# Performance work log

Hardware: AMD Instinct MI355X
Metric: run time of the kernel (lower is better)

Reference implementation:

```python
import jax, jax.numpy as jnp
import numpy as np

B, S, DM = 2, 4096, 512
H, D = 8, 64          # heads, size_per_head
BS = 64               # block size (from == to)
NB = S // BS          # 64 blocks
R = 3                 # num random blocks per middle row


def setup_inputs() -> dict:
    key = jax.random.key(0)
    ks = jax.random.split(key, 8)
    sc = 0.02
    x = jax.random.normal(ks[0], (B, S, DM), dtype=jnp.float32)
    w_q = jax.random.normal(ks[1], (DM, H * D), dtype=jnp.float32) * sc
    b_q = jnp.zeros((H * D,), dtype=jnp.float32)
    w_k = jax.random.normal(ks[2], (DM, H * D), dtype=jnp.float32) * sc
    b_k = jnp.zeros((H * D,), dtype=jnp.float32)
    w_v = jax.random.normal(ks[3], (DM, H * D), dtype=jnp.float32) * sc
    b_v = jnp.zeros((H * D,), dtype=jnp.float32)
    # random attention adjacency: per head, rows 1..NB-2, r random middle blocks
    rand_attn = jax.random.randint(ks[4], (H, NB - 2, R), 1, NB - 1, dtype=jnp.int32)
    return {"x": x, "w_q": w_q, "b_q": b_q, "w_k": w_k, "b_k": b_k,
            "w_v": w_v, "b_v": b_v, "rand_attn": rand_attn}


def _bigbird_attention(q, k, v, rand_attn):
    # q,k,v: [B,H,S,D]; rand_attn: [H,NB-2,R]
    scale = 1.0 / jnp.sqrt(jnp.asarray(D, q.dtype))
    qb = q.reshape(B, H, NB, BS, D)
    kb = k.reshape(B, H, NB, BS, D)
    vb = v.reshape(B, H, NB, BS, D)

    # gather random key/value blocks per head/row: [B,H,NB-2,R*BS,D]
    h_idx = jnp.arange(H)[:, None, None]
    gk = kb[:, h_idx, rand_attn].reshape(B, H, NB - 2, R * BS, D)
    gv = vb[:, h_idx, rand_attn].reshape(B, H, NB - 2, R * BS, D)

    # --- row 0: global, full attention ---
    s0 = jnp.einsum('bhqd,bhkd->bhqk', qb[:, :, 0], k) * scale
    c0 = jnp.einsum('bhqk,bhkd->bhqd', jax.nn.softmax(s0, axis=-1), v)

    # --- row 1: blocks [0,1,2,last] + rand ---
    k1 = jnp.concatenate([kb[:, :, 0], kb[:, :, 1], kb[:, :, 2],
                          kb[:, :, -1], gk[:, :, 0]], axis=2)
    v1 = jnp.concatenate([vb[:, :, 0], vb[:, :, 1], vb[:, :, 2],
                          vb[:, :, -1], gv[:, :, 0]], axis=2)
    s1 = jnp.einsum('bhqd,bhkd->bhqk', qb[:, :, 1], k1) * scale
    c1 = jnp.einsum('bhqk,bhkd->bhqd', jax.nn.softmax(s1, axis=-1), v1)

    # --- middle rows i = 2 .. NB-3: first + band(i-1,i,i+1) + rand + last ---
    q_mid = qb[:, :, 2:NB - 2]                                  # [B,H,M,BS,D]
    band_k = jnp.concatenate([kb[:, :, 1:NB - 3], kb[:, :, 2:NB - 2],
                              kb[:, :, 3:NB - 1]], axis=3)       # [B,H,M,3BS,D]
    band_v = jnp.concatenate([vb[:, :, 1:NB - 3], vb[:, :, 2:NB - 2],
                              vb[:, :, 3:NB - 1]], axis=3)
    gk_mid = gk[:, :, 1:NB - 3]                                  # [B,H,M,R*BS,D]
    gv_mid = gv[:, :, 1:NB - 3]
    s_first = jnp.einsum('bhmqd,bhkd->bhmqk', q_mid, kb[:, :, 0])
    s_band = jnp.einsum('bhmqd,bhmkd->bhmqk', q_mid, band_k)
    s_rand = jnp.einsum('bhmqd,bhmkd->bhmqk', q_mid, gk_mid)
    s_last = jnp.einsum('bhmqd,bhkd->bhmqk', q_mid, kb[:, :, -1])
    s_mid = jnp.concatenate([s_first, s_band, s_rand, s_last], axis=-1) * scale
    p = jax.nn.softmax(s_mid, axis=-1)
    p_first = p[..., :BS]
    p_band = p[..., BS:4 * BS]
    p_rand = p[..., 4 * BS:4 * BS + R * BS]
    p_last = p[..., 4 * BS + R * BS:]
    c_mid = (jnp.einsum('bhmqk,bhkd->bhmqd', p_first, vb[:, :, 0])
             + jnp.einsum('bhmqk,bhmkd->bhmqd', p_band, band_v)
             + jnp.einsum('bhmqk,bhmkd->bhmqd', p_rand, gv_mid)
             + jnp.einsum('bhmqk,bhkd->bhmqd', p_last, vb[:, :, -1]))

    # --- row NB-2: blocks [0, NB-3, NB-2, last] + rand ---
    k2 = jnp.concatenate([kb[:, :, 0], kb[:, :, -3], kb[:, :, -2],
                          kb[:, :, -1], gk[:, :, -1]], axis=2)
    v2 = jnp.concatenate([vb[:, :, 0], vb[:, :, -3], vb[:, :, -2],
                          vb[:, :, -1], gv[:, :, -1]], axis=2)
    s2 = jnp.einsum('bhqd,bhkd->bhqk', qb[:, :, -2], k2) * scale
    c2 = jnp.einsum('bhqk,bhkd->bhqd', jax.nn.softmax(s2, axis=-1), v2)

    # --- last row: global, full attention ---
    s3 = jnp.einsum('bhqd,bhkd->bhqk', qb[:, :, -1], k) * scale
    c3 = jnp.einsum('bhqk,bhkd->bhqd', jax.nn.softmax(s3, axis=-1), v)

    ctx = jnp.concatenate([c0[:, :, None], c1[:, :, None], c_mid,
                           c2[:, :, None], c3[:, :, None]], axis=2)
    return ctx.reshape(B, H, S, D)


def reference(x, w_q, b_q, w_k, b_k, w_v, b_v, rand_attn):
    q = (x @ w_q + b_q).reshape(B, S, H, D).transpose(0, 2, 1, 3)
    k = (x @ w_k + b_k).reshape(B, S, H, D).transpose(0, 2, 1, 3)
    v = (x @ w_v + b_v).reshape(B, S, H, D).transpose(0, 2, 1, 3)
    ctx = _bigbird_attention(q, k, v, rand_attn)  # [B,H,S,D]
    return ctx.transpose(0, 2, 1, 3).reshape(B, S, H * D)
```

## Files before the change

kernel.cpp:

```cpp
#include <hip/hip_runtime.h>
#include <stdint.h>

#define BB 2
#define SS 4096
#define DM 512
#define HH 8
#define DD 64
#define NB 64
#define RR 3

typedef __attribute__((ext_vector_type(8))) short short8;
typedef __attribute__((ext_vector_type(4))) float f4;

__device__ __forceinline__ unsigned short f2bf(float f) {
    unsigned u = __float_as_uint(f);
    unsigned r = (u + 0x7fffu + ((u >> 16) & 1u)) >> 16;
    return (unsigned short)r;
}

__global__ __launch_bounds__(256) void cvt_kernel(
    const float* __restrict__ x,
    const float* __restrict__ wq,
    const float* __restrict__ wk,
    const float* __restrict__ wv,
    unsigned short* __restrict__ xb,
    unsigned short* __restrict__ wbT)
{
    int tid = blockIdx.x * blockDim.x + threadIdx.x;
    const int NX4 = (BB * SS * DM) / 4;
    if (tid < NX4) {
        float4 v = reinterpret_cast<const float4*>(x)[tid];
        ushort4 o;
        o.x = f2bf(v.x); o.y = f2bf(v.y); o.z = f2bf(v.z); o.w = f2bf(v.w);
        reinterpret_cast<ushort4*>(xb)[tid] = o;
    }
    const int NW = 3 * DM * DM;
    if (tid < NW) {
        int n = tid >> 9;
        int k = tid & 511;
        int which = n >> 9;
        int hd = n & 511;
        const float* w = (which == 0) ? wq : (which == 1) ? wk : wv;
        wbT[tid] = f2bf(w[k * DM + hd]);
    }
}

__global__ __launch_bounds__(256) void qkv_gemm(
    const unsigned short* __restrict__ xb,
    const unsigned short* __restrict__ wbT,
    const float* __restrict__ bq,
    const float* __restrict__ bk,
    const float* __restrict__ bv,
    unsigned short* __restrict__ qb,
    unsigned short* __restrict__ kb,
    unsigned short* __restrict__ vT)
{
    __shared__ __attribute__((aligned(16))) unsigned short As[128 * 64];
    __shared__ __attribute__((aligned(16))) unsigned short Bs[128 * 64];
    const int tid = threadIdx.x;
    const int l = tid & 63;
    const int w = tid >> 6;
    const int wr = w >> 1, wc = w & 1;
    const int lq = l & 15, lg = l >> 4;
    const int bid = blockIdx.x;
    const int tn = bid % 12, tm = bid / 12;

    f4 acc[4][4];
#pragma unroll
    for (int m = 0; m < 4; m++)
#pragma unroll
        for (int n = 0; n < 4; n++) acc[m][n] = (f4){0.f, 0.f, 0.f, 0.f};

    for (int kt = 0; kt < 8; ++kt) {
#pragma unroll
        for (int i = 0; i < 4; ++i) {
            int o = i * 4096 + tid * 16;
            int row = o >> 7;
            int g = (o >> 4) & 7;
            short8 va = *reinterpret_cast<const short8*>(
                xb + (size_t)(tm * 128 + row) * DM + kt * 64 + g * 8);
            short8 vb = *reinterpret_cast<const short8*>(
                wbT + (size_t)(tn * 128 + row) * DM + kt * 64 + g * 8);
            int gs = g ^ (row & 7);
            *reinterpret_cast<short8*>(reinterpret_cast<char*>(As) + row * 128 + gs * 16) = va;
            *reinterpret_cast<short8*>(reinterpret_cast<char*>(Bs) + row * 128 + gs * 16) = vb;
        }
        __syncthreads();
#pragma unroll
        for (int c = 0; c < 2; c++) {
            short8 af[4], bf[4];
#pragma unroll
            for (int m = 0; m < 4; m++) {
                int row = wr * 64 + m * 16 + lq;
                int gs = (c * 4 + lg) ^ (row & 7);
                af[m] = *reinterpret_cast<const short8*>(
                    reinterpret_cast<const char*>(As) + row * 128 + gs * 16);
            }
#pragma unroll
            for (int n = 0; n < 4; n++) {
                int row = wc * 64 + n * 16 + lq;
                int gs = (c * 4 + lg) ^ (row & 7);
                bf[n] = *reinterpret_cast<const short8*>(
                    reinterpret_cast<const char*>(Bs) + row * 128 + gs * 16);
            }
#pragma unroll
            for (int m = 0; m < 4; m++)
#pragma unroll
                for (int n = 0; n < 4; n++)
                    acc[m][n] = __builtin_amdgcn_mfma_f32_16x16x32_bf16(af[m], bf[n], acc[m][n], 0, 0, 0);
        }
        __syncthreads();
    }

#pragma unroll
    for (int m = 0; m < 4; m++) {
        int gm = tm * 128 + wr * 64 + m * 16 + lg * 4;
#pragma unroll
        for (int n = 0; n < 4; n++) {
            int gn = tn * 128 + wc * 64 + n * 16 + lq;
            int which = gn >> 9, hd = gn & 511;
            float bias = ((which == 0) ? bq : (which == 1) ? bk : bv)[hd];
            int h = hd >> 6, d = hd & 63;
#pragma unroll
            for (int r = 0; r < 4; r++) {
                int gmr = gm + r;
                int b = gmr >> 12, s = gmr & 4095;
                unsigned short val = f2bf(acc[m][n][r] + bias);
                if (which == 0)
                    qb[(((size_t)b * HH + h) * SS + s) * DD + d] = val;
                else if (which == 1)
                    kb[(((size_t)b * HH + h) * SS + s) * DD + d] = val;
                else
                    vT[(((size_t)b * HH + h) * DD + d) * SS + s] = val;
            }
        }
    }
}

__global__ __launch_bounds__(256) void bigbird_attn(
    const unsigned short* __restrict__ qb,
    const unsigned short* __restrict__ kb,
    const unsigned short* __restrict__ vT,
    const int* __restrict__ rand_attn,
    float* __restrict__ out,
    float* __restrict__ PO,
    float* __restrict__ PL)
{
    __shared__ __attribute__((aligned(16))) unsigned short Kb[2][4096];
    __shared__ __attribute__((aligned(16))) unsigned short Vb[2][4096];
    __shared__ __attribute__((aligned(16))) unsigned short Pl[4][1024];
    const int tid = threadIdx.x;
    const int l = tid & 63, w = tid >> 6;
    const int lq = l & 15, lg = l >> 4;
    const int bid = blockIdx.x;

    int b, h, qi, e = 0, c = 0;
    int kbl[8];
    float bias7 = 0.f;
    bool partial;
    if (bid < 992) {
        partial = false;
        qi = 1 + bid % 62;
        int t = bid / 62;
        h = t & 7;
        b = t >> 3;
        kbl[0] = 0;
        if (qi == 1)       { kbl[1] = 1;  kbl[2] = 2;  kbl[3] = 63; }
        else if (qi == 62) { kbl[1] = 61; kbl[2] = 62; kbl[3] = 63; }
        else               { kbl[1] = qi - 1; kbl[2] = qi; kbl[3] = qi + 1; }
        const int* ra = rand_attn + (h * 62 + (qi - 1)) * 3;
        kbl[4] = ra[0]; kbl[5] = ra[1]; kbl[6] = ra[2];
        if (qi == 1 || qi == 62) { kbl[7] = 0; bias7 = -30.f; }
        else kbl[7] = 63;
    } else {
        partial = true;
        int idx = bid - 992;
        c = idx & 7;
        e = (idx >> 3) & 1;
        h = (idx >> 4) & 7;
        b = idx >> 7;
        qi = e ? 63 : 0;
#pragma unroll
        for (int i = 0; i < 8; ++i) kbl[i] = c * 8 + i;
    }

    const size_t bh = (size_t)b * HH + h;
    const unsigned short* qp = qb + bh * SS * DD;
    const char* kpB = reinterpret_cast<const char*>(kb + bh * SS * DD);
    const char* vpB = reinterpret_cast<const char*>(vT + bh * (size_t)DD * SS);

    const int qrow = qi * 64 + w * 16 + lq;
    short8 qf[2];
#pragma unroll
    for (int cc = 0; cc < 2; cc++)
        qf[cc] = *reinterpret_cast<const short8*>(qp + (size_t)qrow * DD + cc * 32 + lg * 8);

    const int r0 = tid >> 3;
    const int sg = tid & 7;
    const int swz0 = (sg ^ (r0 & 7)) << 4;

#define STAGE_LOAD(blk)                                                                 \
    st0 = *reinterpret_cast<const short8*>(kpB + (size_t)(blk) * 8192 + r0 * 128 + sg * 16);        \
    st1 = *reinterpret_cast<const short8*>(kpB + (size_t)(blk) * 8192 + (r0 + 32) * 128 + sg * 16); \
    st2 = *reinterpret_cast<const short8*>(vpB + (size_t)r0 * 8192 + (size_t)(blk) * 128 + sg * 16);\
    st3 = *reinterpret_cast<const short8*>(vpB + (size_t)(r0 + 32) * 8192 + (size_t)(blk) * 128 + sg * 16);

#define STAGE_WRITE(bb)                                                                  \
    *reinterpret_cast<short8*>(reinterpret_cast<char*>(Kb[bb]) + r0 * 128 + swz0) = st0;             \
    *reinterpret_cast<short8*>(reinterpret_cast<char*>(Kb[bb]) + (r0 + 32) * 128 + swz0) = st1;      \
    *reinterpret_cast<short8*>(reinterpret_cast<char*>(Vb[bb]) + r0 * 128 + swz0) = st2;             \
    *reinterpret_cast<short8*>(reinterpret_cast<char*>(Vb[bb]) + (r0 + 32) * 128 + swz0) = st3;

    short8 st0, st1, st2, st3;
    STAGE_LOAD(kbl[0]);
    STAGE_WRITE(0);
    __syncthreads();

    float lacc[4] = {0.f, 0.f, 0.f, 0.f};
    f4 oacc[4];
#pragma unroll
    for (int g = 0; g < 4; g++) oacc[g] = (f4){0.f, 0.f, 0.f, 0.f};

    char* pb = reinterpret_cast<char*>(&Pl[w][0]);
    const float scale = 0.125f;

#pragma unroll
    for (int i = 0; i < 8; ++i) {
        const int cur = i & 1, nxt = cur ^ 1;
        if (i < 7) { STAGE_LOAD(kbl[i + 1]); }
        const float bi = (i == 7) ? bias7 : 0.f;
        const char* Kc = reinterpret_cast<const char*>(Kb[cur]);
        const char* Vc = reinterpret_cast<const char*>(Vb[cur]);

        f4 sacc[4];
#pragma unroll
        for (int g = 0; g < 4; g++) sacc[g] = (f4){0.f, 0.f, 0.f, 0.f};
#pragma unroll
        for (int cc = 0; cc < 2; cc++) {
#pragma unroll
            for (int g = 0; g < 4; g++) {
                int row = g * 16 + lq;
                short8 kf = *reinterpret_cast<const short8*>(
                    Kc + row * 128 + (((cc * 4 + lg) ^ (row & 7)) << 4));
                sacc[g] = __builtin_amdgcn_mfma_f32_16x16x32_bf16(qf[cc], kf, sacc[g], 0, 0, 0);
            }
        }

#pragma unroll
        for (int g = 0; g < 4; g++)
#pragma unroll
            for (int r = 0; r < 4; r++) {
                float pv = __expf(fmaf(sacc[g][r], scale, bi));
                lacc[r] += pv;
                int row = lg * 4 + r;
                int colbyte = (g * 16 + lq) * 2;
                int gr = (colbyte >> 4) ^ (row & 7);
                *reinterpret_cast<unsigned short*>(pb + row * 128 + (gr << 4) + (colbyte & 15)) =
                    f2bf(pv);
            }

        short8 pa[2];
#pragma unroll
        for (int cc = 0; cc < 2; cc++) {
            int row = lq;
            int gr = (cc * 4 + lg) ^ (row & 7);
            pa[cc] = *reinterpret_cast<const short8*>(pb + row * 128 + (gr << 4));
        }

#pragma unroll
        for (int cc = 0; cc < 2; cc++)
#pragma unroll
            for (int g = 0; g < 4; g++) {
                int row = g * 16 + lq;
                short8 vf = *reinterpret_cast<const short8*>(
                    Vc + row * 128 + (((cc * 4 + lg) ^ (row & 7)) << 4));
                oacc[g] = __builtin_amdgcn_mfma_f32_16x16x32_bf16(pa[cc], vf, oacc[g], 0, 0, 0);
            }

        __syncthreads();
        if (i < 7) { STAGE_WRITE(nxt); }
        __syncthreads();
    }

#pragma unroll
    for (int off = 1; off < 16; off <<= 1)
#pragma unroll
        for (int r = 0; r < 4; r++) lacc[r] += __shfl_xor(lacc[r], off, 64);

    if (!partial) {
#pragma unroll
        for (int r = 0; r < 4; r++) {
            float inv = 1.0f / lacc[r];
            int row = lg * 4 + r;
            int s = qi * 64 + w * 16 + row;
#pragma unroll
            for (int g = 0; g < 4; g++) {
                int d = g * 16 + lq;
                out[((size_t)b * SS + s) * DM + h * DD + d] = oacc[g][r] * inv;
            }
        }
    } else {
        int pr = ((b * 8 + h) * 2 + e);
        float* po = PO + ((size_t)(pr * 8 + c) << 12);
        float* pl = PL + (pr * 8 + c) * 64;
#pragma unroll
        for (int r = 0; r < 4; r++) {
            int row = w * 16 + lg * 4 + r;
#pragma unroll
            for (int g = 0; g < 4; g++)
                po[row * 64 + g * 16 + lq] = oacc[g][r];
            if (lq == 0) pl[row] = lacc[r];
        }
    }
#undef STAGE_LOAD
#undef STAGE_WRITE
}

__global__ __launch_bounds__(256) void bigbird_combine(
    const float* __restrict__ PO,
    const float* __restrict__ PL,
    float* __restrict__ out)
{
    int pr = blockIdx.x;
    int e = pr & 1, h = (pr >> 1) & 7, b = pr >> 4;
    int t = threadIdx.x;
    int row = t >> 2;
    int d0 = (t & 3) * 16;

    float acc[16];
#pragma unroll
    for (int j = 0; j < 16; j++) acc[j] = 0.f;
    float lsum = 0.f;

#pragma unroll
    for (int c = 0; c < 8; c++) {
        const float* po = PO + ((size_t)(pr * 8 + c) << 12) + row * 64 + d0;
#pragma unroll
        for (int j = 0; j < 4; j++) {
            float4 v = *reinterpret_cast<const float4*>(po + j * 4);
            acc[j * 4 + 0] += v.x; acc[j * 4 + 1] += v.y;
            acc[j * 4 + 2] += v.z; acc[j * 4 + 3] += v.w;
        }
        lsum += PL[(pr * 8 + c) * 64 + row];
    }

    int qi = e ? 63 : 0;
    int s = qi * 64 + row;
    float inv = 1.0f / lsum;
    float* op = out + ((size_t)b * SS + s) * DM + h * DD + d0;
#pragma unroll
    for (int j = 0; j < 4; j++) {
        float4 v;
        v.x = acc[j * 4 + 0] * inv; v.y = acc[j * 4 + 1] * inv;
        v.z = acc[j * 4 + 2] * inv; v.w = acc[j * 4 + 3] * inv;
        *reinterpret_cast<float4*>(op + j * 4) = v;
    }
}

extern "C" void kernel_launch(void* const* d_in, const int* in_sizes, int n_in,
                              void* d_out, int out_size, void* d_ws, size_t ws_size,
                              hipStream_t stream) {
    const float* x  = (const float*)d_in[0];
    const float* wq = (const float*)d_in[1];
    const float* bq = (const float*)d_in[2];
    const float* wk = (const float*)d_in[3];
    const float* bk = (const float*)d_in[4];
    const float* wv = (const float*)d_in[5];
    const float* bv = (const float*)d_in[6];
    const int* rand_attn = (const int*)d_in[7];
    float* out = (float*)d_out;

    char* ws = (char*)d_ws;
    unsigned short* xb  = (unsigned short*)ws;
    unsigned short* wbT = (unsigned short*)(ws + 8388608);
    unsigned short* qbp = (unsigned short*)(ws + 9961472);
    unsigned short* kbp = qbp + (size_t)4194304;
    unsigned short* vTp = kbp + (size_t)4194304;
    float* PO = (float*)(ws + 35127296);
    float* PL = (float*)(ws + 35127296 + 4194304);

    hipLaunchKernelGGL(cvt_kernel, dim3(4096), dim3(256), 0, stream, x, wq, wk, wv, xb, wbT);
    hipLaunchKernelGGL(qkv_gemm, dim3(768), dim3(256), 0, stream, xb, wbT, bq, bk, bv, qbp, kbp, vTp);
    hipLaunchKernelGGL(bigbird_attn, dim3(1248), dim3(256), 0, stream, qbp, kbp, vTp, rand_attn, out, PO, PL);
    hipLaunchKernelGGL(bigbird_combine, dim3(32), dim3(256), 0, stream, PO, PL, out);
}
```

Baseline: 158.4 us.

## Use direct global-to-LDS loads, tiled weight transpose, and XCD-aware block remapping

```diff
diff --git a/kernel.cpp b/kernel.cpp
--- a/kernel.cpp
+++ b/kernel.cpp
@@ -16,6 +16,12 @@
     unsigned u = __float_as_uint(f);
     unsigned r = (u + 0x7fffu + ((u >> 16) & 1u)) >> 16;
     return (unsigned short)r;
+}
+
+__device__ __forceinline__ void g2l16(const void* g, void* l) {
+    __builtin_amdgcn_global_load_lds(
+        (const __attribute__((address_space(1))) unsigned int*)g,
+        (__attribute__((address_space(3))) unsigned int*)l, 16, 0, 0);
 }
 
 __global__ __launch_bounds__(256) void cvt_kernel(
@@ -26,22 +32,44 @@
     unsigned short* __restrict__ xb,
     unsigned short* __restrict__ wbT)
 {
-    int tid = blockIdx.x * blockDim.x + threadIdx.x;
-    const int NX4 = (BB * SS * DM) / 4;
-    if (tid < NX4) {
-        float4 v = reinterpret_cast<const float4*>(x)[tid];
-        ushort4 o;
-        o.x = f2bf(v.x); o.y = f2bf(v.y); o.z = f2bf(v.z); o.w = f2bf(v.w);
-        reinterpret_cast<ushort4*>(xb)[tid] = o;
-    }
-    const int NW = 3 * DM * DM;
-    if (tid < NW) {
-        int n = tid >> 9;
-        int k = tid & 511;
-        int which = n >> 9;
-        int hd = n & 511;
+    __shared__ unsigned short Ts[64][68];
+    const int t = threadIdx.x;
+    const int bid = blockIdx.x;
+    if (bid < 2048) {
+        int i0 = bid * 512 + t;
+#pragma unroll
+        for (int p = 0; p < 2; ++p) {
+            float4 v = reinterpret_cast<const float4*>(x)[i0 + p * 256];
+            ushort4 o;
+            o.x = f2bf(v.x); o.y = f2bf(v.y); o.z = f2bf(v.z); o.w = f2bf(v.w);
+            reinterpret_cast<ushort4*>(xb)[i0 + p * 256] = o;
+        }
+    } else {
+        int bid2 = bid - 2048;
+        int which = bid2 >> 6;
+        int tile = bid2 & 63;
+        int tr = tile >> 3, tc = tile & 7;
         const float* w = (which == 0) ? wq : (which == 1) ? wk : wv;
-        wbT[tid] = f2bf(w[k * DM + hd]);
+        int r = t >> 2, c0 = (t & 3) * 16;
+        const float* src = w + (size_t)(tr * 64 + r) * 512 + tc * 64 + c0;
+#pragma unroll
+        for (int j = 0; j < 4; ++j) {
+            float4 v = *reinterpret_cast<const float4*>(src + j * 4);
+            Ts[r][c0 + j * 4 + 0] = f2bf(v.x);
+            Ts[r][c0 + j * 4 + 1] = f2bf(v.y);
+            Ts[r][c0 + j * 4 + 2] = f2bf(v.z);
+            Ts[r][c0 + j * 4 + 3] = f2bf(v.w);
+        }
+        __syncthreads();
+        unsigned short* dst = wbT + (size_t)(which * 512 + tc * 64 + r) * 512 + tr * 64 + c0;
+        short8 o0, o1;
+#pragma unroll
+        for (int j = 0; j < 8; ++j) {
+            ((unsigned short*)&o0)[j] = Ts[c0 + j][r];
+            ((unsigned short*)&o1)[j] = Ts[c0 + 8 + j][r];
+        }
+        *reinterpret_cast<short8*>(dst) = o0;
+        *reinterpret_cast<short8*>(dst + 8) = o1;
     }
 }
 
@@ -63,7 +91,15 @@
     const int wr = w >> 1, wc = w & 1;
     const int lq = l & 15, lg = l >> 4;
     const int bid = blockIdx.x;
-    const int tn = bid % 12, tm = bid / 12;
+    const int rb = (bid & 7) * 96 + (bid >> 3);
+    const int tn = rb % 12, tm = rb / 12;
+
+    const int srow = l >> 3;
+    const int sg = (l & 7) ^ srow;
+    const unsigned short* ag = xb + (size_t)(tm * 128 + w * 32 + srow) * DM + sg * 8;
+    const unsigned short* bg = wbT + (size_t)(tn * 128 + w * 32 + srow) * DM + sg * 8;
+    char* al = reinterpret_cast<char*>(As) + w * 4096;
+    char* bl = reinterpret_cast<char*>(Bs) + w * 4096;
 
     f4 acc[4][4];
 #pragma unroll
@@ -73,17 +109,9 @@
 
     for (int kt = 0; kt < 8; ++kt) {
 #pragma unroll
-        for (int i = 0; i < 4; ++i) {
-            int o = i * 4096 + tid * 16;
-            int row = o >> 7;
-            int g = (o >> 4) & 7;
-            short8 va = *reinterpret_cast<const short8*>(
-                xb + (size_t)(tm * 128 + row) * DM + kt * 64 + g * 8);
-            short8 vb = *reinterpret_cast<const short8*>(
-                wbT + (size_t)(tn * 128 + row) * DM + kt * 64 + g * 8);
-            int gs = g ^ (row & 7);
-            *reinterpret_cast<short8*>(reinterpret_cast<char*>(As) + row * 128 + gs * 16) = va;
-            *reinterpret_cast<short8*>(reinterpret_cast<char*>(Bs) + row * 128 + gs * 16) = vb;
+        for (int j = 0; j < 4; ++j) {
+            g2l16(ag + (size_t)j * 8 * DM + kt * 64, al + j * 1024);
+            g2l16(bg + (size_t)j * 8 * DM + kt * 64, bl + j * 1024);
         }
         __syncthreads();
 #pragma unroll
@@ -152,7 +180,8 @@
     const int tid = threadIdx.x;
     const int l = tid & 63, w = tid >> 6;
     const int lq = l & 15, lg = l >> 4;
-    const int bid = blockIdx.x;
+    const int bid0 = blockIdx.x;
+    const int bid = (bid0 & 7) * 156 + (bid0 >> 3);
 
     int b, h, qi, e = 0, c = 0;
     int kbl[8];
@@ -195,25 +224,22 @@
     for (int cc = 0; cc < 2; cc++)
         qf[cc] = *reinterpret_cast<const short8*>(qp + (size_t)qrow * DD + cc * 32 + lg * 8);
 
-    const int r0 = tid >> 3;
-    const int sg = tid & 7;
-    const int swz0 = (sg ^ (r0 & 7)) << 4;
-
-#define STAGE_LOAD(blk)                                                                 \
-    st0 = *reinterpret_cast<const short8*>(kpB + (size_t)(blk) * 8192 + r0 * 128 + sg * 16);        \
-    st1 = *reinterpret_cast<const short8*>(kpB + (size_t)(blk) * 8192 + (r0 + 32) * 128 + sg * 16); \
-    st2 = *reinterpret_cast<const short8*>(vpB + (size_t)r0 * 8192 + (size_t)(blk) * 128 + sg * 16);\
-    st3 = *reinterpret_cast<const short8*>(vpB + (size_t)(r0 + 32) * 8192 + (size_t)(blk) * 128 + sg * 16);
-
-#define STAGE_WRITE(bb)                                                                  \
-    *reinterpret_cast<short8*>(reinterpret_cast<char*>(Kb[bb]) + r0 * 128 + swz0) = st0;             \
-    *reinterpret_cast<short8*>(reinterpret_cast<char*>(Kb[bb]) + (r0 + 32) * 128 + swz0) = st1;      \
-    *reinterpret_cast<short8*>(reinterpret_cast<char*>(Vb[bb]) + r0 * 128 + swz0) = st2;             \
-    *reinterpret_cast<short8*>(reinterpret_cast<char*>(Vb[bb]) + (r0 + 32) * 128 + swz0) = st3;
-
-    short8 st0, st1, st2, st3;
-    STAGE_LOAD(kbl[0]);
-    STAGE_WRITE(0);
+    const int srow = l >> 3;
+    const int sg = (l & 7) ^ srow;
+
+#define STAGE(bufidx, blk)                                                              \
+    {                                                                                   \
+        const char* kq = kpB + (size_t)(blk) * 8192;                                    \
+        const char* vq = vpB + (size_t)(blk) * 128;                                     \
+        char* kl = reinterpret_cast<char*>(Kb[bufidx]) + w * 2048;                      \
+        char* vl = reinterpret_cast<char*>(Vb[bufidx]) + w * 2048;                      \
+        g2l16(kq + (w * 16 + srow) * 128 + sg * 16, kl);                                \
+        g2l16(kq + (w * 16 + 8 + srow) * 128 + sg * 16, kl + 1024);                     \
+        g2l16(vq + (size_t)(w * 16 + srow) * 8192 + sg * 16, vl);                       \
+        g2l16(vq + (size_t)(w * 16 + 8 + srow) * 8192 + sg * 16, vl + 1024);            \
+    }
+
+    STAGE(0, kbl[0]);
     __syncthreads();
 
     float lacc[4] = {0.f, 0.f, 0.f, 0.f};
@@ -226,8 +252,8 @@
 
 #pragma unroll
     for (int i = 0; i < 8; ++i) {
-        const int cur = i & 1, nxt = cur ^ 1;
-        if (i < 7) { STAGE_LOAD(kbl[i + 1]); }
+        const int cur = i & 1;
+        if (i < 7) { STAGE(cur ^ 1, kbl[i + 1]); }
         const float bi = (i == 7) ? bias7 : 0.f;
         const char* Kc = reinterpret_cast<const char*>(Kb[cur]);
         const char* Vc = reinterpret_cast<const char*>(Vb[cur]);
@@ -278,9 +304,8 @@
             }
 
         __syncthreads();
-        if (i < 7) { STAGE_WRITE(nxt); }
-        __syncthreads();
-    }
+    }
+#undef STAGE
 
 #pragma unroll
     for (int off = 1; off < 16; off <<= 1)
@@ -312,8 +337,6 @@
             if (lq == 0) pl[row] = lacc[r];
         }
     }
-#undef STAGE_LOAD
-#undef STAGE_WRITE
 }
 
 __global__ __launch_bounds__(256) void bigbird_combine(
@@ -379,7 +402,7 @@
     float* PO = (float*)(ws + 35127296);
     float* PL = (float*)(ws + 35127296 + 4194304);
 
-    hipLaunchKernelGGL(cvt_kernel, dim3(4096), dim3(256), 0, stream, x, wq, wk, wv, xb, wbT);
+    hipLaunchKernelGGL(cvt_kernel, dim3(2240), dim3(256), 0, stream, x, wq, wk, wv, xb, wbT);
     hipLaunchKernelGGL(qkv_gemm, dim3(768), dim3(256), 0, stream, xb, wbT, bq, bk, bv, qbp, kbp, vTp);
     hipLaunchKernelGGL(bigbird_attn, dim3(1248), dim3(256), 0, stream, qbp, kbp, vTp, rand_attn, out, PO, PL);
     hipLaunchKernelGGL(bigbird_combine, dim3(32), dim3(256), 0, stream, PO, PL, out);
```

After: 140.1 us. 1.13x faster.
